# Optimization experiments

Hardware: AMD Instinct MI355X
Metric: run time of the kernel (lower is better)

Reference implementation:

```python
import jax, jax.numpy as jnp
import numpy as np

N = 20000
E = 320000
D = 256
OUT = 256
NEG_SLOPE = 0.2


def setup_inputs() -> dict:
    key = jax.random.key(0)
    ks = jax.random.split(key, 16)
    s = 1.0 / np.sqrt(D)
    x = jax.random.normal(ks[0], (N, D), dtype=jnp.float32)
    edge_index = jax.random.randint(ks[1], (2, E), 0, N, dtype=jnp.int64)
    W1 = jax.random.uniform(ks[2], (D, D), jnp.float32, -s, s)
    W2 = jax.random.uniform(ks[3], (D, D), jnp.float32, -s, s)
    Ws = jax.random.uniform(ks[4], (6, D, D), jnp.float32, -s, s)      # per-layer GATConv lin weight
    a_src = jax.random.uniform(ks[5], (6, D), jnp.float32, -s, s)      # per-layer att_src
    a_dst = jax.random.uniform(ks[6], (6, D), jnp.float32, -s, s)      # per-layer att_dst
    bias = jnp.zeros((6, D), dtype=jnp.float32)                        # per-layer GATConv bias
    W3 = jax.random.uniform(ks[7], (2 * D, OUT), jnp.float32, -s, s)
    return {"x": x, "edge_index": edge_index, "W1": W1, "W2": W2,
            "Ws": Ws, "a_src": a_src, "a_dst": a_dst, "bias": bias, "W3": W3}


def _gat_layer(h, src, dst, W, asrc, adst, b):
    # h: [N, D] -> linear transform
    hw = h @ W                                         # [N, D]
    e_src = hw @ asrc                                  # [N]
    e_dst = hw @ adst                                  # [N]
    e = jax.nn.leaky_relu(e_src[src] + e_dst[dst], NEG_SLOPE)  # [E]
    # softmax over incoming edges per destination node
    m = jax.ops.segment_max(e, dst, num_segments=N)    # [N], -inf for empty segs (unused)
    ee = jnp.exp(e - m[dst])                           # [E]
    denom = jax.ops.segment_sum(ee, dst, num_segments=N)
    alpha = ee / denom[dst]                            # [E]
    msg = alpha[:, None] * hw[src]                     # [E, D]
    out = jax.ops.segment_sum(msg, dst, num_segments=N)  # [N, D]
    return out + b


def reference(x, edge_index, W1, W2, Ws, a_src, a_dst, bias, W3):
    src, dst = edge_index[0], edge_index[1]
    h = x @ W1
    h = h @ W2
    for i in range(6):
        h = _gat_layer(h, src, dst, Ws[i], a_src[i], a_dst[i], bias[i])
    h = jnp.concatenate((h, h), axis=1)   # [N, 2D]
    h = jax.nn.relu(h)
    return h @ W3                          # [N, OUT]
```

## Files before the change

kernel.cpp:

```cpp
#include <hip/hip_runtime.h>
#include <hip/hip_fp16.h>
#include <stdint.h>

#define NNODES 20000
#define EEDGES 320000
#define DD     256
#define NEG_SLOPE 0.2f
#define SCAN_BLOCKS ((NNODES + 255) / 256)
#define ESTR   20480

typedef _Float16 half8 __attribute__((ext_vector_type(8)));
typedef _Float16 half4 __attribute__((ext_vector_type(4)));
typedef float f32x4 __attribute__((ext_vector_type(4)));


__global__ void zero_ints_k(int* __restrict__ p, int n) {
    int i = blockIdx.x * 256 + threadIdx.x;
    if (i < n) p[i] = 0;
}

__global__ void hist_k(const int* __restrict__ dst, int* __restrict__ rowptr) {
    int i = blockIdx.x * 256 + threadIdx.x;
    if (i < EEDGES) atomicAdd(&rowptr[dst[i] + 1], 1);
}

__global__ __launch_bounds__(256) void scan1_k(int* __restrict__ rowptr, int* __restrict__ bsums) {
    __shared__ int buf[256];
    int idx = blockIdx.x * 256 + threadIdx.x;
    int v = (idx < NNODES) ? rowptr[idx + 1] : 0;
    buf[threadIdx.x] = v;
    __syncthreads();
#pragma unroll
    for (int off = 1; off < 256; off <<= 1) {
        int t = (threadIdx.x >= (unsigned)off) ? buf[threadIdx.x - off] : 0;
        __syncthreads();
        buf[threadIdx.x] += t;
        __syncthreads();
    }
    if (idx < NNODES) rowptr[idx + 1] = buf[threadIdx.x];
    if (threadIdx.x == 255) bsums[blockIdx.x] = buf[255];
}

__global__ __launch_bounds__(128) void scan2_k(int* __restrict__ bsums) {
    __shared__ int buf[128];
    int v = (threadIdx.x < SCAN_BLOCKS) ? bsums[threadIdx.x] : 0;
    buf[threadIdx.x] = v;
    __syncthreads();
#pragma unroll
    for (int off = 1; off < 128; off <<= 1) {
        int t = (threadIdx.x >= (unsigned)off) ? buf[threadIdx.x - off] : 0;
        __syncthreads();
        buf[threadIdx.x] += t;
        __syncthreads();
    }
    if (threadIdx.x < SCAN_BLOCKS) bsums[threadIdx.x] = buf[threadIdx.x];
}

__global__ void scan3_k(int* __restrict__ rowptr, const int* __restrict__ bsums,
                        int* __restrict__ cursor) {
    int idx = blockIdx.x * 256 + threadIdx.x;
    if (idx < NNODES) {
        int v = rowptr[idx + 1];
        if (blockIdx.x > 0) { v += bsums[blockIdx.x - 1]; rowptr[idx + 1] = v; }
        if (idx + 1 < NNODES) cursor[idx + 1] = v;
        if (idx == 0) cursor[0] = 0;
    }
}

__global__ void scatter_k(const int* __restrict__ src, const int* __restrict__ dst,
                          int* __restrict__ cursor, int* __restrict__ colsrc) {
    int i = blockIdx.x * 256 + threadIdx.x;
    if (i < EEDGES) {
        int d = dst[i];
        int pos = atomicAdd(&cursor[d], 1);
        colsrc[pos] = src[i];
    }
}


__global__ void cvt_split_k(const float* __restrict__ X, _Float16* __restrict__ Xh,
                            _Float16* __restrict__ Xl, int n) {
    int i = blockIdx.x * 256 + threadIdx.x;
    if (i < n) {
        float v = X[i];
        _Float16 hi = (_Float16)v;
        Xh[i] = hi;
        Xl[i] = (_Float16)(v - (float)hi);
    }
}


template<bool SUM>
__global__ void cvt_w_k(const float* __restrict__ W, _Float16* __restrict__ Wh,
                        _Float16* __restrict__ Wl) {
    int i = blockIdx.x * 256 + threadIdx.x;
    if (i < DD * DD) {
        int k = i >> 8, n = i & 255;
        float v = W[i];
        if (SUM) v += W[i + DD * DD];
        _Float16 hi = (_Float16)v;
        Wh[n * DD + k] = hi;
        Wl[n * DD + k] = (_Float16)(v - (float)hi);
    }
}


template<bool OUT_SPLIT, bool DOTS>
__global__ __launch_bounds__(512, 4) void gemm_k(
    const _Float16* __restrict__ Ah, const _Float16* __restrict__ Al,
    const _Float16* __restrict__ Bh, const _Float16* __restrict__ Bl,
    float* __restrict__ C, _Float16* __restrict__ Ch, _Float16* __restrict__ Cl,
    const float* __restrict__ asrc, const float* __restrict__ adst,
    float* __restrict__ esp, float* __restrict__ edp, int M)
{
    __shared__ _Float16 smem[24576];
    _Float16* sAh = smem;
    _Float16* sAl = smem + 4096;
    _Float16* sBh = smem + 8192;
    _Float16* sBl = smem + 16384;

    const int t = threadIdx.x;
    const int lane = t & 63;
    const int w = t >> 6;
    const int rowBase = blockIdx.y * 64;
    const int colBase = blockIdx.x * 128;
    const int mo = (w & 1) * 32;
    const int no = (w >> 1) * 32;

    const int arow = t >> 3;
    const int slot = t & 7;
    const int swz = (slot ^ (arow & 7)) << 3;

    f32x4 acc[2][2];
#pragma unroll
    for (int m = 0; m < 2; ++m)
#pragma unroll
        for (int n = 0; n < 2; ++n) acc[m][n] = (f32x4){0.f, 0.f, 0.f, 0.f};

    int4 pa_h, pa_l, pb_h0, pb_h1, pb_l0, pb_l1;

#define LOADSTAGE(S) { \
        size_t aoff  = (size_t)(rowBase + arow) * DD + (S) * 64 + slot * 8; \
        size_t boff0 = (size_t)(colBase + arow) * DD + (S) * 64 + slot * 8; \
        size_t boff1 = boff0 + (size_t)64 * DD; \
        pa_h  = *(const int4*)(Ah + aoff); \
        pa_l  = *(const int4*)(Al + aoff); \
        pb_h0 = *(const int4*)(Bh + boff0); \
        pb_h1 = *(const int4*)(Bh + boff1); \
        pb_l0 = *(const int4*)(Bl + boff0); \
        pb_l1 = *(const int4*)(Bl + boff1); \
    }

#define WRITESTAGE() { \
        int da  = arow * 64 + swz; \
        *(int4*)(sAh + da) = pa_h; \
        *(int4*)(sAl + da) = pa_l; \
        *(int4*)(sBh + da) = pb_h0; \
        *(int4*)(sBh + da + 4096) = pb_h1; \
        *(int4*)(sBl + da) = pb_l0; \
        *(int4*)(sBl + da + 4096) = pb_l1; \
    }

    LOADSTAGE(0);
    const int fr = lane & 15;
    const int fq = lane >> 4;

    for (int s = 0; s < 4; ++s) {
        __syncthreads();
        WRITESTAGE();
        __syncthreads();
        if (s < 3) { LOADSTAGE(s + 1); }

#pragma unroll
        for (int kk = 0; kk < 2; ++kk) {
            const int c = kk * 4 + fq;
            half8 ah[2], al[2], bh[2], bl[2];
#pragma unroll
            for (int m = 0; m < 2; ++m) {
                int ra = mo + m * 16 + fr;
                int oa = ra * 64 + ((c ^ (ra & 7)) << 3);
                ah[m] = *(const half8*)(sAh + oa);
                al[m] = *(const half8*)(sAl + oa);
            }
#pragma unroll
            for (int n = 0; n < 2; ++n) {
                int rb = no + n * 16 + fr;
                int ob = rb * 64 + ((c ^ (rb & 7)) << 3);
                bh[n] = *(const half8*)(sBh + ob);
                bl[n] = *(const half8*)(sBl + ob);
            }
#pragma unroll
            for (int m = 0; m < 2; ++m)
#pragma unroll
                for (int n = 0; n < 2; ++n) {
                    acc[m][n] = __builtin_amdgcn_mfma_f32_16x16x32_f16(ah[m], bh[n], acc[m][n], 0, 0, 0);
                    acc[m][n] = __builtin_amdgcn_mfma_f32_16x16x32_f16(ah[m], bl[n], acc[m][n], 0, 0, 0);
                    acc[m][n] = __builtin_amdgcn_mfma_f32_16x16x32_f16(al[m], bh[n], acc[m][n], 0, 0, 0);
                    acc[m][n] = __builtin_amdgcn_mfma_f32_16x16x32_f16(al[m], bl[n], acc[m][n], 0, 0, 0);
                }
        }
    }
#undef LOADSTAGE
#undef WRITESTAGE

    const int ccol = lane & 15;
    const int crq = (lane >> 4) * 4;

    if constexpr (OUT_SPLIT) {
        __syncthreads();
#pragma unroll
        for (int m = 0; m < 2; ++m)
#pragma unroll
            for (int n = 0; n < 2; ++n)
#pragma unroll
                for (int r = 0; r < 4; ++r) {
                    int row = mo + m * 16 + crq + r;
                    int col = no + n * 16 + ccol;
                    float v = acc[m][n][r];
                    _Float16 hi = (_Float16)v;
                    smem[row * 136 + col] = hi;
                    smem[8704 + row * 136 + col] = (_Float16)(v - (float)hi);
                }
        __syncthreads();
#pragma unroll
        for (int i = 0; i < 2; ++i) {
            int slotId = i * 512 + t;
            int srow = slotId >> 4;
            int sc = slotId & 15;
            int grow = rowBase + srow;
            if (grow < M) {
                half8 hv = *(const half8*)(smem + srow * 136 + sc * 8);
                half8 lv = *(const half8*)(smem + 8704 + srow * 136 + sc * 8);
                *(half8*)(Ch + (size_t)grow * DD + colBase + sc * 8) = hv;
                *(half8*)(Cl + (size_t)grow * DD + colBase + sc * 8) = lv;
            }
        }
    } else {
#pragma unroll
        for (int m = 0; m < 2; ++m) {
            int growb = rowBase + mo + m * 16 + crq;
#pragma unroll
            for (int n = 0; n < 2; ++n) {
                int gcol = colBase + no + n * 16 + ccol;
#pragma unroll
                for (int r = 0; r < 4; ++r) {
                    int grow = growb + r;
                    if (grow < M) C[(size_t)grow * DD + gcol] = acc[m][n][r];
                }
            }
        }
    }

    if constexpr (DOTS) {
        float as0 = asrc[colBase + no + ccol];
        float as1 = asrc[colBase + no + 16 + ccol];
        float ad0 = adst[colBase + no + ccol];
        float ad1 = adst[colBase + no + 16 + ccol];
        __syncthreads();
        float* sred = (float*)smem;
        const int cw = w >> 1;
#pragma unroll
        for (int m = 0; m < 2; ++m)
#pragma unroll
            for (int r = 0; r < 4; ++r) {
                float ps = acc[m][0][r] * as0 + acc[m][1][r] * as1;
                float pd = acc[m][0][r] * ad0 + acc[m][1][r] * ad1;
#pragma unroll
                for (int off = 1; off < 16; off <<= 1) {
                    ps += __shfl_xor(ps, off);
                    pd += __shfl_xor(pd, off);
                }
                if (ccol == 0) {
                    int row = mo + m * 16 + crq + r;
                    sred[row * 8 + cw] = ps;
                    sred[512 + row * 8 + cw] = pd;
                }
            }
        __syncthreads();
        if (t < 64) {
            float esb = sred[t * 8 + 0] + sred[t * 8 + 1] + sred[t * 8 + 2] + sred[t * 8 + 3];
            float edb = sred[512 + t * 8 + 0] + sred[512 + t * 8 + 1]
                      + sred[512 + t * 8 + 2] + sred[512 + t * 8 + 3];
            int grow = rowBase + t;
            if (grow < M) {
                esp[(size_t)blockIdx.x * ESTR + grow] = esb;
                edp[(size_t)blockIdx.x * ESTR + grow] = edb;
            }
        }
    }
}


template<bool RELU>
__global__ __launch_bounds__(256) void gat_agg_k(const float* __restrict__ hw,
                                                 const float* __restrict__ es0,
                                                 const float* __restrict__ es1,
                                                 const float* __restrict__ ed0,
                                                 const float* __restrict__ ed1,
                                                 const int* __restrict__ rowptr,
                                                 const int* __restrict__ colsrc,
                                                 float* __restrict__ ealpha,
                                                 const float* __restrict__ bias,
                                                 _Float16* __restrict__ hh,
                                                 _Float16* __restrict__ hl) {
    int wave = threadIdx.x >> 6;
    int lane = threadIdx.x & 63;
    int node = blockIdx.x * 4 + wave;
    if (node >= NNODES) return;
    int start = rowptr[node], end = rowptr[node + 1];
    int deg = end - start;
    float edd = ed0[node] + ed1[node];

    float4 acc0 = make_float4(0.f, 0.f, 0.f, 0.f);
    float4 acc1 = acc0, acc2 = acc0, acc3 = acc0;

#define FMA4(ACC, W_, V) \
    ACC.x = fmaf(W_, V.x, ACC.x); ACC.y = fmaf(W_, V.y, ACC.y); \
    ACC.z = fmaf(W_, V.z, ACC.z); ACC.w = fmaf(W_, V.w, ACC.w);

    if (deg > 0 && deg <= 64) {
        bool valid = lane < deg;
        int msrc = valid ? colsrc[start + lane] : 0;
        float e = valid ? es0[msrc] + es1[msrc] + edd : -INFINITY;
        e = fmaxf(e, NEG_SLOPE * e);
        float mx = e;
#pragma unroll
        for (int off = 32; off; off >>= 1) mx = fmaxf(mx, __shfl_xor(mx, off));
        float ee = valid ? expf(e - mx) : 0.f;
        float sum = ee;
#pragma unroll
        for (int off = 32; off; off >>= 1) sum += __shfl_xor(sum, off);
        float w = ee / sum;

#define FETCH8(V, W_, JB) \
        _Pragma("unroll") \
        for (int q = 0; q < 8; ++q) { \
            int sq = __shfl(msrc, (JB) + q); \
            W_[q] = __shfl(w, (JB) + q); \
            V[q] = *(const float4*)(hw + (size_t)sq * DD + lane * 4); \
        }

#define FMA8(V, W_) \
        FMA4(acc0, W_[0], V[0]); FMA4(acc1, W_[1], V[1]); \
        FMA4(acc2, W_[2], V[2]); FMA4(acc3, W_[3], V[3]); \
        FMA4(acc0, W_[4], V[4]); FMA4(acc1, W_[5], V[5]); \
        FMA4(acc2, W_[6], V[6]); FMA4(acc3, W_[7], V[7]);

        const int nfull = deg & ~7;
        if (nfull > 0) {
            float4 va[8], vb[8];
            float wa[8], wb[8];
            FETCH8(va, wa, 0);
            int jb = 8;
            for (;;) {
                if (jb >= nfull) { FMA8(va, wa); break; }
                FETCH8(vb, wb, jb); jb += 8;
                __builtin_amdgcn_sched_barrier(0);
                FMA8(va, wa);
                if (jb >= nfull) { FMA8(vb, wb); break; }
                FETCH8(va, wa, jb); jb += 8;
                __builtin_amdgcn_sched_barrier(0);
                FMA8(vb, wb);
            }
        }
        int j2 = nfull;
        if (j2 + 4 <= deg) {
            int s0 = __shfl(msrc, j2 + 0), s1 = __shfl(msrc, j2 + 1);
            int s2 = __shfl(msrc, j2 + 2), s3 = __shfl(msrc, j2 + 3);
            float w0 = __shfl(w, j2 + 0), w1 = __shfl(w, j2 + 1);
            float w2 = __shfl(w, j2 + 2), w3 = __shfl(w, j2 + 3);
            float4 v0 = *(const float4*)(hw + (size_t)s0 * DD + lane * 4);
            float4 v1 = *(const float4*)(hw + (size_t)s1 * DD + lane * 4);
            float4 v2 = *(const float4*)(hw + (size_t)s2 * DD + lane * 4);
            float4 v3 = *(const float4*)(hw + (size_t)s3 * DD + lane * 4);
            FMA4(acc0, w0, v0); FMA4(acc1, w1, v1);
            FMA4(acc2, w2, v2); FMA4(acc3, w3, v3);
            j2 += 4;
        }
        for (; j2 < deg; ++j2) {
            int   s0 = __shfl(msrc, j2);
            float w0 = __shfl(w, j2);
            float4 v0 = *(const float4*)(hw + (size_t)s0 * DD + lane * 4);
            FMA4(acc0, w0, v0);
        }
#undef FETCH8
#undef FMA8
    } else if (deg > 64) {
        float mx = -INFINITY;
        for (int j = start + lane; j < end; j += 64) {
            int s = colsrc[j];
            float e = es0[s] + es1[s] + edd;
            e = fmaxf(e, NEG_SLOPE * e);
            mx = fmaxf(mx, e);
        }
#pragma unroll
        for (int off = 32; off; off >>= 1) mx = fmaxf(mx, __shfl_xor(mx, off));
        float sum = 0.f;
        for (int j = start + lane; j < end; j += 64) {
            int s = colsrc[j];
            float e = es0[s] + es1[s] + edd;
            e = fmaxf(e, NEG_SLOPE * e);
            float ee = expf(e - mx);
            ealpha[j] = ee;
            sum += ee;
        }
#pragma unroll
        for (int off = 32; off; off >>= 1) sum += __shfl_xor(sum, off);
        float inv = 1.f / sum;
        int j = start;
        for (; j + 4 <= end; j += 4) {
            int s0 = colsrc[j], s1 = colsrc[j + 1], s2 = colsrc[j + 2], s3 = colsrc[j + 3];
            float w0 = ealpha[j] * inv, w1 = ealpha[j + 1] * inv;
            float w2 = ealpha[j + 2] * inv, w3 = ealpha[j + 3] * inv;
            float4 v0 = *(const float4*)(hw + (size_t)s0 * DD + lane * 4);
            float4 v1 = *(const float4*)(hw + (size_t)s1 * DD + lane * 4);
            float4 v2 = *(const float4*)(hw + (size_t)s2 * DD + lane * 4);
            float4 v3 = *(const float4*)(hw + (size_t)s3 * DD + lane * 4);
            FMA4(acc0, w0, v0); FMA4(acc1, w1, v1);
            FMA4(acc2, w2, v2); FMA4(acc3, w3, v3);
        }
        for (; j < end; ++j) {
            int s0 = colsrc[j];
            float w0 = ealpha[j] * inv;
            float4 v0 = *(const float4*)(hw + (size_t)s0 * DD + lane * 4);
            FMA4(acc0, w0, v0);
        }
    }
#undef FMA4

    acc0.x += acc1.x; acc0.y += acc1.y; acc0.z += acc1.z; acc0.w += acc1.w;
    acc2.x += acc3.x; acc2.y += acc3.y; acc2.z += acc3.z; acc2.w += acc3.w;
    acc0.x += acc2.x; acc0.y += acc2.y; acc0.z += acc2.z; acc0.w += acc2.w;
    float4 b4 = *(const float4*)(bias + lane * 4);
    acc0.x += b4.x; acc0.y += b4.y; acc0.z += b4.z; acc0.w += b4.w;
    if (RELU) {
        acc0.x = fmaxf(acc0.x, 0.f); acc0.y = fmaxf(acc0.y, 0.f);
        acc0.z = fmaxf(acc0.z, 0.f); acc0.w = fmaxf(acc0.w, 0.f);
    }
    size_t base = (size_t)node * DD + lane * 4;
    _Float16 h0 = (_Float16)acc0.x, h1 = (_Float16)acc0.y;
    _Float16 h2 = (_Float16)acc0.z, h3 = (_Float16)acc0.w;
    half4 hv; hv[0] = h0; hv[1] = h1; hv[2] = h2; hv[3] = h3;
    half4 lv;
    lv[0] = (_Float16)(acc0.x - (float)h0); lv[1] = (_Float16)(acc0.y - (float)h1);
    lv[2] = (_Float16)(acc0.z - (float)h2); lv[3] = (_Float16)(acc0.w - (float)h3);
    *(half4*)(hh + base) = hv;
    *(half4*)(hl + base) = lv;
}


extern "C" void kernel_launch(void* const* d_in, const int* in_sizes, int n_in,
                              void* d_out, int out_size, void* d_ws, size_t ws_size,
                              hipStream_t stream) {
    const float* x     = (const float*)d_in[0];
    const int*   ei    = (const int*)d_in[1];
    const float* W1    = (const float*)d_in[2];
    const float* W2    = (const float*)d_in[3];
    const float* Ws    = (const float*)d_in[4];
    const float* a_src = (const float*)d_in[5];
    const float* a_dst = (const float*)d_in[6];
    const float* bias  = (const float*)d_in[7];
    const float* W3    = (const float*)d_in[8];
    float* out = (float*)d_out;

    const int* src = ei;
    const int* dst = ei + EEDGES;

    const size_t ND = (size_t)NNODES * DD;

    float* bufA   = (float*)d_ws;
    float* es01   = bufA + ND;
    float* ed01   = es01 + 2 * ESTR;
    float* ealpha = ed01 + 2 * ESTR;
    int*   rowptr = (int*)(ealpha + EEDGES);
    int*   cursor = rowptr + (NNODES + 1);
    int*   colsrc = cursor + NNODES;
    int*   bsums  = colsrc + EEDGES;
    _Float16* P0h = (_Float16*)(((uintptr_t)(bsums + SCAN_BLOCKS) + 15) & ~(uintptr_t)15);
    _Float16* P0l = P0h + ND;
    _Float16* P1h = P0l + ND;
    _Float16* P1l = P1h + ND;
    _Float16* WT  = P1l + ND;
    const size_t WSZ = (size_t)DD * DD;

    zero_ints_k<<<(NNODES + 1 + 255) / 256, 256, 0, stream>>>(rowptr, NNODES + 1);
    hist_k<<<(EEDGES + 255) / 256, 256, 0, stream>>>(dst, rowptr);
    scan1_k<<<SCAN_BLOCKS, 256, 0, stream>>>(rowptr, bsums);
    scan2_k<<<1, 128, 0, stream>>>(bsums);
    scan3_k<<<SCAN_BLOCKS, 256, 0, stream>>>(rowptr, bsums, cursor);
    scatter_k<<<(EEDGES + 255) / 256, 256, 0, stream>>>(src, dst, cursor, colsrc);

    const int WBLK = (DD * DD + 255) / 256;
    cvt_w_k<false><<<WBLK, 256, 0, stream>>>(W1, WT + 0 * 2 * WSZ, WT + 0 * 2 * WSZ + WSZ);
    cvt_w_k<false><<<WBLK, 256, 0, stream>>>(W2, WT + 1 * 2 * WSZ, WT + 1 * 2 * WSZ + WSZ);
    for (int l = 0; l < 6; ++l)
        cvt_w_k<false><<<WBLK, 256, 0, stream>>>(Ws + (size_t)l * WSZ,
                                                 WT + (2 + l) * 2 * WSZ,
                                                 WT + (2 + l) * 2 * WSZ + WSZ);
    cvt_w_k<true><<<WBLK, 256, 0, stream>>>(W3, WT + 8 * 2 * WSZ, WT + 8 * 2 * WSZ + WSZ);

    cvt_split_k<<<(int)((ND + 255) / 256), 256, 0, stream>>>(x, P0h, P0l, (int)ND);

    dim3 gg(DD / 128, (NNODES + 63) / 64);
    const int nodeBlocks = (NNODES + 3) / 4;

#define WTH(i) (WT + (i) * 2 * WSZ)
#define WTL(i) (WT + (i) * 2 * WSZ + WSZ)

    gemm_k<true, false><<<gg, 512, 0, stream>>>(P0h, P0l, WTH(0), WTL(0), nullptr, P1h, P1l,
                                                nullptr, nullptr, nullptr, nullptr, NNODES);
    gemm_k<true, false><<<gg, 512, 0, stream>>>(P1h, P1l, WTH(1), WTL(1), nullptr, P0h, P0l,
                                                nullptr, nullptr, nullptr, nullptr, NNODES);

    for (int l = 0; l < 6; ++l) {
        gemm_k<false, true><<<gg, 512, 0, stream>>>(P0h, P0l, WTH(2 + l), WTL(2 + l),
                                                    bufA, nullptr, nullptr,
                                                    a_src + (size_t)l * DD, a_dst + (size_t)l * DD,
                                                    es01, ed01, NNODES);
        if (l < 5)
            gat_agg_k<false><<<nodeBlocks, 256, 0, stream>>>(bufA, es01, es01 + ESTR,
                                                             ed01, ed01 + ESTR,
                                                             rowptr, colsrc, ealpha,
                                                             bias + (size_t)l * DD, P0h, P0l);
        else
            gat_agg_k<true><<<nodeBlocks, 256, 0, stream>>>(bufA, es01, es01 + ESTR,
                                                            ed01, ed01 + ESTR,
                                                            rowptr, colsrc, ealpha,
                                                            bias + (size_t)l * DD, P0h, P0l);
    }

    gemm_k<false, false><<<gg, 512, 0, stream>>>(P0h, P0l, WTH(8), WTL(8), out,
                                                 nullptr, nullptr,
                                                 nullptr, nullptr, nullptr, nullptr, NNODES);
#undef WTH
#undef WTL
}
```

Before: 641.3 us.

## Precompute W1@W2 product and simplify small-degree GAT aggregation loop

The two leading dense GEMMs over all nodes (x@W1 then @W2) become one: W1·W2 is multiplied once as a small 256x256 GEMM into a new weight slot, and x is multiplied by that product. This removes a full N×D×D GEMM pass at the cost of a tiny extra GEMM and a slightly different rounding order. The small-degree aggregation path also replaces the hand-pipelined double-buffered fetch with a plain 8-wide unrolled loop using eight accumulators, leaving load scheduling to the compiler.

```diff
diff --git a/kernel.cpp b/kernel.cpp
--- a/kernel.cpp
+++ b/kernel.cpp
@@ -313,79 +313,72 @@
 
     float4 acc0 = make_float4(0.f, 0.f, 0.f, 0.f);
     float4 acc1 = acc0, acc2 = acc0, acc3 = acc0;
+    float4 acc4 = acc0, acc5 = acc0, acc6 = acc0, acc7 = acc0;
 
 #define FMA4(ACC, W_, V) \
     ACC.x = fmaf(W_, V.x, ACC.x); ACC.y = fmaf(W_, V.y, ACC.y); \
     ACC.z = fmaf(W_, V.z, ACC.z); ACC.w = fmaf(W_, V.w, ACC.w);
 
-    if (deg > 0 && deg <= 64) {
-        bool valid = lane < deg;
-        int msrc = valid ? colsrc[start + lane] : 0;
-        float e = valid ? es0[msrc] + es1[msrc] + edd : -INFINITY;
-        e = fmaxf(e, NEG_SLOPE * e);
-        float mx = e;
-#pragma unroll
-        for (int off = 32; off; off >>= 1) mx = fmaxf(mx, __shfl_xor(mx, off));
-        float ee = valid ? expf(e - mx) : 0.f;
-        float sum = ee;
-#pragma unroll
-        for (int off = 32; off; off >>= 1) sum += __shfl_xor(sum, off);
-        float w = ee / sum;
-
-#define FETCH8(V, W_, JB) \
-        _Pragma("unroll") \
-        for (int q = 0; q < 8; ++q) { \
-            int sq = __shfl(msrc, (JB) + q); \
-            W_[q] = __shfl(w, (JB) + q); \
-            V[q] = *(const float4*)(hw + (size_t)sq * DD + lane * 4); \
-        }
-
-#define FMA8(V, W_) \
-        FMA4(acc0, W_[0], V[0]); FMA4(acc1, W_[1], V[1]); \
-        FMA4(acc2, W_[2], V[2]); FMA4(acc3, W_[3], V[3]); \
-        FMA4(acc0, W_[4], V[4]); FMA4(acc1, W_[5], V[5]); \
-        FMA4(acc2, W_[6], V[6]); FMA4(acc3, W_[7], V[7]);
-
-        const int nfull = deg & ~7;
-        if (nfull > 0) {
-            float4 va[8], vb[8];
-            float wa[8], wb[8];
-            FETCH8(va, wa, 0);
-            int jb = 8;
-            for (;;) {
-                if (jb >= nfull) { FMA8(va, wa); break; }
-                FETCH8(vb, wb, jb); jb += 8;
-                __builtin_amdgcn_sched_barrier(0);
-                FMA8(va, wa);
-                if (jb >= nfull) { FMA8(vb, wb); break; }
-                FETCH8(va, wa, jb); jb += 8;
-                __builtin_amdgcn_sched_barrier(0);
-                FMA8(vb, wb);
-            }
-        }
-        int j2 = nfull;
-        if (j2 + 4 <= deg) {
-            int s0 = __shfl(msrc, j2 + 0), s1 = __shfl(msrc, j2 + 1);
-            int s2 = __shfl(msrc, j2 + 2), s3 = __shfl(msrc, j2 + 3);
-            float w0 = __shfl(w, j2 + 0), w1 = __shfl(w, j2 + 1);
-            float w2 = __shfl(w, j2 + 2), w3 = __shfl(w, j2 + 3);
-            float4 v0 = *(const float4*)(hw + (size_t)s0 * DD + lane * 4);
-            float4 v1 = *(const float4*)(hw + (size_t)s1 * DD + lane * 4);
-            float4 v2 = *(const float4*)(hw + (size_t)s2 * DD + lane * 4);
-            float4 v3 = *(const float4*)(hw + (size_t)s3 * DD + lane * 4);
-            FMA4(acc0, w0, v0); FMA4(acc1, w1, v1);
-            FMA4(acc2, w2, v2); FMA4(acc3, w3, v3);
-            j2 += 4;
-        }
-        for (; j2 < deg; ++j2) {
-            int   s0 = __shfl(msrc, j2);
-            float w0 = __shfl(w, j2);
-            float4 v0 = *(const float4*)(hw + (size_t)s0 * DD + lane * 4);
-            FMA4(acc0, w0, v0);
-        }
-#undef FETCH8
-#undef FMA8
-    } else if (deg > 64) {
+    if (deg <= 64) {
+        if (deg > 0) {
+            int j = start + lane;
+            bool valid = j < end;
+            int msrc = valid ? colsrc[j] : 0;
+            float e = valid ? es0[msrc] + es1[msrc] + edd : -INFINITY;
+            e = fmaxf(e, NEG_SLOPE * e);
+            float mx = e;
+#pragma unroll
+            for (int off = 32; off; off >>= 1) mx = fmaxf(mx, __shfl_xor(mx, off));
+            float ee = valid ? expf(e - mx) : 0.f;
+            float sum = ee;
+#pragma unroll
+            for (int off = 32; off; off >>= 1) sum += __shfl_xor(sum, off);
+            float w = ee / sum;
+
+            int j2 = 0;
+            for (; j2 + 8 <= deg; j2 += 8) {
+                int s0 = __shfl(msrc, j2 + 0), s1 = __shfl(msrc, j2 + 1);
+                int s2 = __shfl(msrc, j2 + 2), s3 = __shfl(msrc, j2 + 3);
+                int s4 = __shfl(msrc, j2 + 4), s5 = __shfl(msrc, j2 + 5);
+                int s6 = __shfl(msrc, j2 + 6), s7 = __shfl(msrc, j2 + 7);
+                float w0 = __shfl(w, j2 + 0), w1 = __shfl(w, j2 + 1);
+                float w2 = __shfl(w, j2 + 2), w3 = __shfl(w, j2 + 3);
+                float w4 = __shfl(w, j2 + 4), w5 = __shfl(w, j2 + 5);
+                float w6 = __shfl(w, j2 + 6), w7 = __shfl(w, j2 + 7);
+                float4 v0 = *(const float4*)(hw + (size_t)s0 * DD + lane * 4);
+                float4 v1 = *(const float4*)(hw + (size_t)s1 * DD + lane * 4);
+                float4 v2 = *(const float4*)(hw + (size_t)s2 * DD + lane * 4);
+                float4 v3 = *(const float4*)(hw + (size_t)s3 * DD + lane * 4);
+                float4 v4 = *(const float4*)(hw + (size_t)s4 * DD + lane * 4);
+                float4 v5 = *(const float4*)(hw + (size_t)s5 * DD + lane * 4);
+                float4 v6 = *(const float4*)(hw + (size_t)s6 * DD + lane * 4);
+                float4 v7 = *(const float4*)(hw + (size_t)s7 * DD + lane * 4);
+                FMA4(acc0, w0, v0); FMA4(acc1, w1, v1);
+                FMA4(acc2, w2, v2); FMA4(acc3, w3, v3);
+                FMA4(acc4, w4, v4); FMA4(acc5, w5, v5);
+                FMA4(acc6, w6, v6); FMA4(acc7, w7, v7);
+            }
+            if (j2 + 4 <= deg) {
+                int s0 = __shfl(msrc, j2 + 0), s1 = __shfl(msrc, j2 + 1);
+                int s2 = __shfl(msrc, j2 + 2), s3 = __shfl(msrc, j2 + 3);
+                float w0 = __shfl(w, j2 + 0), w1 = __shfl(w, j2 + 1);
+                float w2 = __shfl(w, j2 + 2), w3 = __shfl(w, j2 + 3);
+                float4 v0 = *(const float4*)(hw + (size_t)s0 * DD + lane * 4);
+                float4 v1 = *(const float4*)(hw + (size_t)s1 * DD + lane * 4);
+                float4 v2 = *(const float4*)(hw + (size_t)s2 * DD + lane * 4);
+                float4 v3 = *(const float4*)(hw + (size_t)s3 * DD + lane * 4);
+                FMA4(acc0, w0, v0); FMA4(acc1, w1, v1);
+                FMA4(acc2, w2, v2); FMA4(acc3, w3, v3);
+                j2 += 4;
+            }
+            for (; j2 < deg; ++j2) {
+                int   s0 = __shfl(msrc, j2);
+                float w0 = __shfl(w, j2);
+                float4 v0 = *(const float4*)(hw + (size_t)s0 * DD + lane * 4);
+                FMA4(acc0, w0, v0);
+            }
+        }
+    } else {
         float mx = -INFINITY;
         for (int j = start + lane; j < end; j += 64) {
             int s = colsrc[j];
@@ -428,6 +421,10 @@
     }
 #undef FMA4
 
+    acc0.x += acc4.x; acc0.y += acc4.y; acc0.z += acc4.z; acc0.w += acc4.w;
+    acc1.x += acc5.x; acc1.y += acc5.y; acc1.z += acc5.z; acc1.w += acc5.w;
+    acc2.x += acc6.x; acc2.y += acc6.y; acc2.z += acc6.z; acc2.w += acc6.w;
+    acc3.x += acc7.x; acc3.y += acc7.y; acc3.z += acc7.z; acc3.w += acc7.w;
     acc0.x += acc1.x; acc0.y += acc1.y; acc0.z += acc1.z; acc0.w += acc1.w;
     acc2.x += acc3.x; acc2.y += acc3.y; acc2.z += acc3.z; acc2.w += acc3.w;
     acc0.x += acc2.x; acc0.y += acc2.y; acc0.z += acc2.z; acc0.w += acc2.w;
@@ -483,6 +480,9 @@
     _Float16* WT  = P1l + ND;
     const size_t WSZ = (size_t)DD * DD;
 
+#define WTH(i) (WT + (i) * 2 * WSZ)
+#define WTL(i) (WT + (i) * 2 * WSZ + WSZ)
+
     zero_ints_k<<<(NNODES + 1 + 255) / 256, 256, 0, stream>>>(rowptr, NNODES + 1);
     hist_k<<<(EEDGES + 255) / 256, 256, 0, stream>>>(dst, rowptr);
     scan1_k<<<SCAN_BLOCKS, 256, 0, stream>>>(rowptr, bsums);
@@ -491,29 +491,27 @@
     scatter_k<<<(EEDGES + 255) / 256, 256, 0, stream>>>(src, dst, cursor, colsrc);
 
     const int WBLK = (DD * DD + 255) / 256;
-    cvt_w_k<false><<<WBLK, 256, 0, stream>>>(W1, WT + 0 * 2 * WSZ, WT + 0 * 2 * WSZ + WSZ);
-    cvt_w_k<false><<<WBLK, 256, 0, stream>>>(W2, WT + 1 * 2 * WSZ, WT + 1 * 2 * WSZ + WSZ);
+    cvt_split_k<<<WBLK, 256, 0, stream>>>(W1, WTH(0), WTL(0), DD * DD);
+    cvt_w_k<false><<<WBLK, 256, 0, stream>>>(W2, WTH(1), WTL(1));
     for (int l = 0; l < 6; ++l)
-        cvt_w_k<false><<<WBLK, 256, 0, stream>>>(Ws + (size_t)l * WSZ,
-                                                 WT + (2 + l) * 2 * WSZ,
-                                                 WT + (2 + l) * 2 * WSZ + WSZ);
-    cvt_w_k<true><<<WBLK, 256, 0, stream>>>(W3, WT + 8 * 2 * WSZ, WT + 8 * 2 * WSZ + WSZ);
+        cvt_w_k<false><<<WBLK, 256, 0, stream>>>(Ws + (size_t)l * WSZ, WTH(2 + l), WTL(2 + l));
+    cvt_w_k<true><<<WBLK, 256, 0, stream>>>(W3, WTH(8), WTL(8));
+
+    dim3 gw(DD / 128, (DD + 63) / 64);
+    gemm_k<true, false><<<gw, 512, 0, stream>>>(WTH(1), WTL(1), WTH(0), WTL(0),
+                                                nullptr, WTH(9), WTL(9),
+                                                nullptr, nullptr, nullptr, nullptr, DD);
 
     cvt_split_k<<<(int)((ND + 255) / 256), 256, 0, stream>>>(x, P0h, P0l, (int)ND);
 
     dim3 gg(DD / 128, (NNODES + 63) / 64);
     const int nodeBlocks = (NNODES + 3) / 4;
 
-#define WTH(i) (WT + (i) * 2 * WSZ)
-#define WTL(i) (WT + (i) * 2 * WSZ + WSZ)
-
-    gemm_k<true, false><<<gg, 512, 0, stream>>>(P0h, P0l, WTH(0), WTL(0), nullptr, P1h, P1l,
+    gemm_k<true, false><<<gg, 512, 0, stream>>>(P0h, P0l, WTH(9), WTL(9), nullptr, P1h, P1l,
                                                 nullptr, nullptr, nullptr, nullptr, NNODES);
-    gemm_k<true, false><<<gg, 512, 0, stream>>>(P1h, P1l, WTH(1), WTL(1), nullptr, P0h, P0l,
-                                                nullptr, nullptr, nullptr, nullptr, NNODES);
 
     for (int l = 0; l < 6; ++l) {
-        gemm_k<false, true><<<gg, 512, 0, stream>>>(P0h, P0l, WTH(2 + l), WTL(2 + l),
+        gemm_k<false, true><<<gg, 512, 0, stream>>>(P1h, P1l, WTH(2 + l), WTL(2 + l),
                                                     bufA, nullptr, nullptr,
                                                     a_src + (size_t)l * DD, a_dst + (size_t)l * DD,
                                                     es01, ed01, NNODES);
@@ -521,15 +519,15 @@
             gat_agg_k<false><<<nodeBlocks, 256, 0, stream>>>(bufA, es01, es01 + ESTR,
                                                              ed01, ed01 + ESTR,
                                                              rowptr, colsrc, ealpha,
-                                                             bias + (size_t)l * DD, P0h, P0l);
+                                                             bias + (size_t)l * DD, P1h, P1l);
         else
             gat_agg_k<true><<<nodeBlocks, 256, 0, stream>>>(bufA, es01, es01 + ESTR,
                                                             ed01, ed01 + ESTR,
                                                             rowptr, colsrc, ealpha,
-                                                            bias + (size_t)l * DD, P0h, P0l);
-    }
-
-    gemm_k<false, false><<<gg, 512, 0, stream>>>(P0h, P0l, WTH(8), WTL(8), out,
+                                                            bias + (size_t)l * DD, P1h, P1l);
+    }
+
+    gemm_k<false, false><<<gg, 512, 0, stream>>>(P1h, P1l, WTH(8), WTL(8), out,
                                                  nullptr, nullptr,
                                                  nullptr, nullptr, nullptr, nullptr, NNODES);
 #undef WTH
```

New measurement: 596.3 us. 1.08x faster.
